# Optimization experiments

Measured on AMD Instinct MI355X. Metric: run time of the kernel, lower is better.

Reference implementation:

```python
import jax, jax.numpy as jnp
import numpy as np

DIM = 256
H = 4
D = DIM // H  # head_dim = 64
SCALE = D ** -0.5


def setup_inputs() -> dict:
    key = jax.random.key(0)
    ks = jax.random.split(key, 12)
    B, N, M = 4, 2048, 2048
    x_query = jax.random.normal(ks[0], (B, N, DIM), dtype=jnp.float32)
    x_context = jax.random.normal(ks[1], (B, M, DIM), dtype=jnp.float32)
    geo_bias = jax.random.normal(ks[2], (B, H, N, M), dtype=jnp.float32)
    init = 1.0 / np.sqrt(DIM)
    Wq = jax.random.uniform(ks[3], (DIM, DIM), jnp.float32, -init, init)
    bq = jax.random.uniform(ks[4], (DIM,), jnp.float32, -init, init)
    Wk = jax.random.uniform(ks[5], (DIM, DIM), jnp.float32, -init, init)
    bk = jax.random.uniform(ks[6], (DIM,), jnp.float32, -init, init)
    Wv = jax.random.uniform(ks[7], (DIM, DIM), jnp.float32, -init, init)
    bv = jax.random.uniform(ks[8], (DIM,), jnp.float32, -init, init)
    Wo = jax.random.uniform(ks[9], (DIM, DIM), jnp.float32, -init, init)
    bo = jax.random.uniform(ks[10], (DIM,), jnp.float32, -init, init)
    return {"x_query": x_query, "x_context": x_context, "geo_bias": geo_bias,
            "Wq": Wq, "bq": bq, "Wk": Wk, "bk": bk, "Wv": Wv, "bv": bv,
            "Wo": Wo, "bo": bo}


def reference(x_query, x_context, geo_bias, Wq, bq, Wk, bk, Wv, bv, Wo, bo):
    B, N, _ = x_query.shape
    M = x_context.shape[1]
    # projections; nn.Linear computes x @ W.T + b
    q = (x_query @ Wq.T + bq).reshape(B, N, H, D).transpose(0, 2, 1, 3)   # (B,H,N,D)
    k = (x_context @ Wk.T + bk).reshape(B, M, H, D).transpose(0, 2, 1, 3)  # (B,H,M,D)
    v = (x_context @ Wv.T + bv).reshape(B, M, H, D).transpose(0, 2, 1, 3)  # (B,H,M,D)
    attn = jnp.einsum("bhnd,bhmd->bhnm", q, k) * SCALE + geo_bias
    attn = jax.nn.softmax(attn, axis=-1)
    out = jnp.einsum("bhnm,bhmd->bhnd", attn, v)
    out = out.transpose(0, 2, 1, 3).reshape(B, N, DIM)
    return out @ Wo.T + bo
```

## Files before the change

### kernel.cpp

```cpp
#include <hip/hip_runtime.h>

typedef unsigned short u16;
typedef unsigned int u32;
using bf16x8  = __attribute__((ext_vector_type(8))) __bf16;
using u16x8   = __attribute__((ext_vector_type(8), may_alias)) u16;
using u16x4   = __attribute__((ext_vector_type(4), may_alias)) u16;
using f32x4   = __attribute__((ext_vector_type(4))) float;
using f32x4_a = __attribute__((ext_vector_type(4), may_alias)) float;

#define DEV __device__ __forceinline__

constexpr int Bn = 4, Hn = 4, Nn = 2048, Mn = 2048, Dn = 64, DIMn = 256;
constexpr float SCALEc = 0.125f;
constexpr float SHIFTc = 12.0f;
constexpr int LSTRIDE = 152;

DEV float bf2f(u16 h) { u32 u = ((u32)h) << 16; return __builtin_bit_cast(float, u); }
DEV u16 f2bf(float f) {
    u32 u = __builtin_bit_cast(u32, f);
    u += 0x7fffu + ((u >> 16) & 1u);
    return (u16)(u >> 16);
}
DEV bf16x8 ld8bf(const u16* p) {
    return __builtin_bit_cast(bf16x8, *reinterpret_cast<const u16x8*>(p));
}
DEV bf16x8 ld8f_bf(const float* p) {
    const f32x4 a = *reinterpret_cast<const f32x4_a*>(p);
    const f32x4 b = *reinterpret_cast<const f32x4_a*>(p + 4);
    u16x8 r;
    r[0] = f2bf(a[0]); r[1] = f2bf(a[1]); r[2] = f2bf(a[2]); r[3] = f2bf(a[3]);
    r[4] = f2bf(b[0]); r[5] = f2bf(b[1]); r[6] = f2bf(b[2]); r[7] = f2bf(b[3]);
    return __builtin_bit_cast(bf16x8, r);
}

__global__ __launch_bounds__(256, 4) void qkv_kernel(
    const float* __restrict__ Xq, const float* __restrict__ Wq, const float* __restrict__ bq,
    const float* __restrict__ Xc, const float* __restrict__ Wk, const float* __restrict__ bk,
    const float* __restrict__ Wv, const float* __restrict__ bv,
    float* __restrict__ Q, u16* __restrict__ K, u16* __restrict__ V)
{
    const int wave = threadIdx.x >> 6, lane = threadIdx.x & 63;
    const int quad = lane >> 4, l16 = lane & 15;
    const int o0 = wave * 64;

    if (blockIdx.x < 512) {
        const int row0 = blockIdx.x * 16;
        const int b = row0 >> 11, n0 = row0 & 2047;
        f32x4 acc[4] = {};
        #pragma unroll
        for (int k0 = 0; k0 < 256; k0 += 32) {
            bf16x8 wf[4];
            const bf16x8 af = ld8f_bf(Xq + (size_t)(row0 + l16) * DIMn + k0 + quad * 8);
            #pragma unroll
            for (int os = 0; os < 4; os++)
                wf[os] = ld8f_bf(Wq + (size_t)(o0 + os * 16 + l16) * DIMn + k0 + quad * 8);
            #pragma unroll
            for (int os = 0; os < 4; os++)
                acc[os] = __builtin_amdgcn_mfma_f32_16x16x32_bf16(af, wf[os], acc[os], 0, 0, 0);
        }
        #pragma unroll
        for (int os = 0; os < 4; os++) {
            const int col = o0 + os * 16 + l16;
            const int h = col >> 6, d = col & 63;
            const float bb = bq[col];
            #pragma unroll
            for (int r = 0; r < 4; r++) {
                const int n = n0 + quad * 4 + r;
                Q[((size_t)(b * Hn + h) * Nn + n) * Dn + d] = acc[os][r] + bb;
            }
        }
    } else {
        const int row0 = (blockIdx.x - 512) * 16;
        const int b = row0 >> 11, n0 = row0 & 2047;
        f32x4 ack[4] = {};
        f32x4 acv[4] = {};
        #pragma unroll
        for (int k0 = 0; k0 < 256; k0 += 32) {
            bf16x8 wkf[4], wvf[4];
            const bf16x8 af = ld8f_bf(Xc + (size_t)(row0 + l16) * DIMn + k0 + quad * 8);
            #pragma unroll
            for (int os = 0; os < 4; os++) {
                wkf[os] = ld8f_bf(Wk + (size_t)(o0 + os * 16 + l16) * DIMn + k0 + quad * 8);
                wvf[os] = ld8f_bf(Wv + (size_t)(o0 + os * 16 + l16) * DIMn + k0 + quad * 8);
            }
            #pragma unroll
            for (int os = 0; os < 4; os++) {
                ack[os] = __builtin_amdgcn_mfma_f32_16x16x32_bf16(af, wkf[os], ack[os], 0, 0, 0);
                acv[os] = __builtin_amdgcn_mfma_f32_16x16x32_bf16(wvf[os], af, acv[os], 0, 0, 0);
            }
        }
        #pragma unroll
        for (int os = 0; os < 4; os++) {
            const int col = o0 + os * 16 + l16;
            const int h = col >> 6, d = col & 63;
            const float bb = bk[col];
            #pragma unroll
            for (int r = 0; r < 4; r++) {
                const int m = n0 + quad * 4 + r;
                K[((size_t)(b * Hn + h) * Mn + m) * Dn + d] = f2bf(ack[os][r] + bb);
            }
        }
        #pragma unroll
        for (int os = 0; os < 4; os++)
            #pragma unroll
            for (int r = 0; r < 4; r++) {
                const int colf = o0 + os * 16 + quad * 4 + r;
                const int h = colf >> 6, d = colf & 63;
                const float bb = bv[colf];
                const int m = n0 + l16;
                V[((size_t)(b * Hn + h) * Dn + d) * Mn + m] = f2bf(acv[os][r] + bb);
            }
    }
}

__global__ __launch_bounds__(256, 4) void attn_kernel(
    const float* __restrict__ Q,
    const u16* __restrict__ K,
    const u16* __restrict__ V,
    const float* __restrict__ geo,
    float* __restrict__ Pnum,
    float* __restrict__ Lsum,
    int S)
{
    __shared__ __align__(16) u16 lds[4][32 * LSTRIDE];

    const int h = blockIdx.y;
    const int b = blockIdx.z / S, split = blockIdx.z % S;
    const int wave = threadIdx.x >> 6, lane = threadIdx.x & 63;
    const int quad = lane >> 4, l16 = lane & 15;
    const int nbase = blockIdx.x * 128 + wave * 32;
    const int mlen = Mn / S, mbeg = split * mlen;

    const float* Qh = Q + ((size_t)(b * Hn + h) * Nn + nbase) * Dn;
    const u16*   Kh = K + (size_t)(b * Hn + h) * Mn * Dn;
    const u16*   Vh = V + (size_t)(b * Hn + h) * Dn * Mn;
    const float* Gq0 = geo + ((size_t)(b * Hn + h) * Nn + nbase + l16) * (size_t)Mn + quad * 4;
    const float* Gq1 = Gq0 + (size_t)16 * Mn;

    bf16x8 qh[2][2], ql[2][2];
    #pragma unroll
    for (int nt = 0; nt < 2; nt++)
        #pragma unroll
        for (int kh = 0; kh < 2; kh++) {
            const float* qp = Qh + (size_t)(nt * 16 + l16) * Dn + kh * 32 + quad * 8;
            const f32x4 a = *reinterpret_cast<const f32x4_a*>(qp);
            const f32x4 c = *reinterpret_cast<const f32x4_a*>(qp + 4);
            u16x8 hi, lo;
            #pragma unroll
            for (int j = 0; j < 4; j++) {
                hi[j] = f2bf(a[j]); lo[j] = f2bf(a[j] - bf2f(hi[j]));
                hi[4 + j] = f2bf(c[j]); lo[4 + j] = f2bf(c[j] - bf2f(hi[4 + j]));
            }
            qh[nt][kh] = __builtin_bit_cast(bf16x8, hi);
            ql[nt][kh] = __builtin_bit_cast(bf16x8, lo);
        }

    f32x4 oacc[2][4] = {};
    float lsum0 = 0.f, lsum1 = 0.f;
    u16* pl = &lds[wave][0];
    const u16* kbase = Kh + (size_t)l16 * Dn + quad * 8;

    for (int m0 = mbeg; m0 < mbeg + mlen; m0 += 128) {
        const u16* kp0 = kbase + (size_t)m0 * Dn;
        bf16x8 kb0 = ld8bf(kp0), kb1 = ld8bf(kp0 + 32);
        f32x4 g0 = *reinterpret_cast<const f32x4_a*>(Gq0 + m0);
        f32x4 g1 = *reinterpret_cast<const f32x4_a*>(Gq1 + m0);
        #pragma unroll
        for (int ms = 0; ms < 8; ms++) {
            bf16x8 nk0, nk1; f32x4 ng0, ng1;
            if (ms < 7) {
                const int mb = m0 + (ms + 1) * 16;
                const u16* kp = kbase + (size_t)mb * Dn;
                nk0 = ld8bf(kp); nk1 = ld8bf(kp + 32);
                ng0 = *reinterpret_cast<const f32x4_a*>(Gq0 + mb);
                ng1 = *reinterpret_cast<const f32x4_a*>(Gq1 + mb);
            }
            f32x4 s0 = {}, s1 = {};
            __builtin_amdgcn_s_setprio(1);
            s0 = __builtin_amdgcn_mfma_f32_16x16x32_bf16(kb0, qh[0][0], s0, 0, 0, 0);
            s1 = __builtin_amdgcn_mfma_f32_16x16x32_bf16(kb0, qh[1][0], s1, 0, 0, 0);
            s0 = __builtin_amdgcn_mfma_f32_16x16x32_bf16(kb0, ql[0][0], s0, 0, 0, 0);
            s1 = __builtin_amdgcn_mfma_f32_16x16x32_bf16(kb0, ql[1][0], s1, 0, 0, 0);
            s0 = __builtin_amdgcn_mfma_f32_16x16x32_bf16(kb1, qh[0][1], s0, 0, 0, 0);
            s1 = __builtin_amdgcn_mfma_f32_16x16x32_bf16(kb1, qh[1][1], s1, 0, 0, 0);
            s0 = __builtin_amdgcn_mfma_f32_16x16x32_bf16(kb1, ql[0][1], s0, 0, 0, 0);
            s1 = __builtin_amdgcn_mfma_f32_16x16x32_bf16(kb1, ql[1][1], s1, 0, 0, 0);
            __builtin_amdgcn_s_setprio(0);
            u16x4 pk0, pk1;
            float ls0 = 0.f, ls1 = 0.f;
            #pragma unroll
            for (int r = 0; r < 4; r++) {
                const float p0 = __expf(fmaf(s0[r], SCALEc, g0[r]) - SHIFTc);
                const float p1 = __expf(fmaf(s1[r], SCALEc, g1[r]) - SHIFTc);
                ls0 += p0; ls1 += p1;
                pk0[r] = f2bf(p0); pk1[r] = f2bf(p1);
            }
            lsum0 += ls0; lsum1 += ls1;
            *reinterpret_cast<u16x4*>(pl + l16 * LSTRIDE + ms * 16 + quad * 4) = pk0;
            *reinterpret_cast<u16x4*>(pl + (16 + l16) * LSTRIDE + ms * 16 + quad * 4) = pk1;
            if (ms < 7) { kb0 = nk0; kb1 = nk1; g0 = ng0; g1 = ng1; }
        }
        const u16* vb0 = Vh + (size_t)l16 * Mn + m0 + quad * 8;
        #pragma unroll
        for (int kh = 0; kh < 4; kh++) {
            const bf16x8 pa0 = ld8bf(pl + l16 * LSTRIDE + kh * 32 + quad * 8);
            const bf16x8 pa1 = ld8bf(pl + (16 + l16) * LSTRIDE + kh * 32 + quad * 8);
            bf16x8 vb[4];
            #pragma unroll
            for (int ds = 0; ds < 4; ds++)
                vb[ds] = ld8bf(vb0 + (size_t)(ds * 16) * Mn + kh * 32);
            __builtin_amdgcn_s_setprio(1);
            #pragma unroll
            for (int ds = 0; ds < 4; ds++) {
                oacc[0][ds] = __builtin_amdgcn_mfma_f32_16x16x32_bf16(pa0, vb[ds], oacc[0][ds], 0, 0, 0);
                oacc[1][ds] = __builtin_amdgcn_mfma_f32_16x16x32_bf16(pa1, vb[ds], oacc[1][ds], 0, 0, 0);
            }
            __builtin_amdgcn_s_setprio(0);
        }
    }

    lsum0 += __shfl_xor(lsum0, 16);
    lsum0 += __shfl_xor(lsum0, 32);
    lsum1 += __shfl_xor(lsum1, 16);
    lsum1 += __shfl_xor(lsum1, 32);

    float* PN = Pnum + (size_t)split * (Bn * (size_t)Nn * DIMn)
                     + ((size_t)b * Nn + nbase) * DIMn + h * Dn;
    #pragma unroll
    for (int nt = 0; nt < 2; nt++)
        #pragma unroll
        for (int r = 0; r < 4; r++)
            #pragma unroll
            for (int ds = 0; ds < 4; ds++)
                PN[(size_t)(nt * 16 + quad * 4 + r) * DIMn + ds * 16 + l16] = oacc[nt][ds][r];

    if (lane < 16) {
        Lsum[(((size_t)split * Bn + b) * Hn + h) * Nn + nbase + l16] = lsum0;
        Lsum[(((size_t)split * Bn + b) * Hn + h) * Nn + nbase + 16 + l16] = lsum1;
    }
}

__global__ __launch_bounds__(256) void combine_kernel(
    const float* __restrict__ Pnum, const float* __restrict__ Lsum,
    u16* __restrict__ AO, int S)
{
    const int idx = blockIdx.x * 256 + threadIdx.x;
    const int row = idx >> 5;
    const int c0  = (idx & 31) * 8;
    const int b = row >> 11, n = row & 2047, h = c0 >> 6;

    float l = 0.f;
    for (int s = 0; s < S; s++)
        l += Lsum[(((size_t)s * Bn + b) * Hn + h) * Nn + n];
    const float inv = 1.0f / l;

    f32x4 a0 = {}, a1 = {};
    for (int s = 0; s < S; s++) {
        const float* p = Pnum + (size_t)s * (Bn * (size_t)Nn * DIMn) + (size_t)row * DIMn + c0;
        a0 += *reinterpret_cast<const f32x4_a*>(p);
        a1 += *reinterpret_cast<const f32x4_a*>(p + 4);
    }
    u16x8 o;
    #pragma unroll
    for (int j = 0; j < 4; j++) {
        o[j]     = f2bf(a0[j] * inv);
        o[4 + j] = f2bf(a1[j] * inv);
    }
    *reinterpret_cast<u16x8*>(AO + (size_t)row * DIMn + c0) = o;
}

__global__ __launch_bounds__(256, 4) void oproj_kernel(
    const u16* __restrict__ A, const float* __restrict__ W,
    const float* __restrict__ bias, float* __restrict__ out)
{
    const int row0 = blockIdx.x * 16;
    const int wave = threadIdx.x >> 6, lane = threadIdx.x & 63;
    const int quad = lane >> 4, l16 = lane & 15;
    const int o0 = wave * 64;

    f32x4 acc[4] = {};
    #pragma unroll
    for (int k0 = 0; k0 < 256; k0 += 32) {
        bf16x8 wf[4];
        const bf16x8 af = ld8bf(A + (size_t)(row0 + l16) * DIMn + k0 + quad * 8);
        #pragma unroll
        for (int os = 0; os < 4; os++)
            wf[os] = ld8f_bf(W + (size_t)(o0 + os * 16 + l16) * DIMn + k0 + quad * 8);
        #pragma unroll
        for (int os = 0; os < 4; os++)
            acc[os] = __builtin_amdgcn_mfma_f32_16x16x32_bf16(af, wf[os], acc[os], 0, 0, 0);
    }
    #pragma unroll
    for (int os = 0; os < 4; os++) {
        const int col = o0 + os * 16 + l16;
        const float bb = bias[col];
        #pragma unroll
        for (int r = 0; r < 4; r++) {
            const int row = row0 + quad * 4 + r;
            out[(size_t)row * DIMn + col] = acc[os][r] + bb;
        }
    }
}

extern "C" void kernel_launch(void* const* d_in, const int* in_sizes, int n_in,
                              void* d_out, int out_size, void* d_ws, size_t ws_size,
                              hipStream_t stream) {
    const float* xq  = (const float*)d_in[0];
    const float* xc  = (const float*)d_in[1];
    const float* geo = (const float*)d_in[2];
    const float* Wq  = (const float*)d_in[3];
    const float* bq  = (const float*)d_in[4];
    const float* Wk  = (const float*)d_in[5];
    const float* bk  = (const float*)d_in[6];
    const float* Wv  = (const float*)d_in[7];
    const float* bv  = (const float*)d_in[8];
    const float* Wo  = (const float*)d_in[9];
    const float* bo  = (const float*)d_in[10];

    const int S = (ws_size >= (60ull << 20)) ? 4 : 1;

    char* ws = (char*)d_ws;
    float* Qw   = (float*)ws;
    u16*   Kw   = (u16*)(ws + (8ull << 20));
    u16*   Vw   = (u16*)(ws + (12ull << 20));
    u16*   AOw  = (u16*)(ws + (16ull << 20));
    float* Pnum = (float*)(ws + (20ull << 20));
    float* Lsum = (float*)(ws + (20ull << 20) + (size_t)S * (8ull << 20));

    qkv_kernel<<<1024, 256, 0, stream>>>(xq, Wq, bq, xc, Wk, bk, Wv, bv, Qw, Kw, Vw);
    attn_kernel<<<dim3(Nn / 128, Hn, Bn * S), 256, 0, stream>>>(Qw, Kw, Vw, geo, Pnum, Lsum, S);
    combine_kernel<<<(Bn * Nn * 32) / 256, 256, 0, stream>>>(Pnum, Lsum, AOw, S);
    oproj_kernel<<<Bn * Nn / 16, 256, 0, stream>>>(AOw, Wo, bo, (float*)d_out);
}
```

Before: 569.4 us.

## Shrink attention tile to 16 rows per wave and fuse split-combine into output projection

The attention kernel now gives each wave 16 query rows instead of 32, which doubles the grid and halves the registers and LDS each block needs. The geo-bias loads for a whole 128-column chunk are now issued in one batch ahead of use. The separate combine kernel is removed: the output projection reads the split partial numerators and sums directly, normalises them and converts them to bf16 in registers. This saves one launch and the AO round trip through memory. In exchange, each K/V tile is loaded twice as often per query row, and the oproj kernel repeats the split reduction for each k-slice.

```diff
diff --git a/kernel.cpp b/kernel.cpp
--- a/kernel.cpp
+++ b/kernel.cpp
@@ -122,170 +122,154 @@
     float* __restrict__ Lsum,
     int S)
 {
-    __shared__ __align__(16) u16 lds[4][32 * LSTRIDE];
+    __shared__ __align__(16) u16 lds[4][16 * LSTRIDE];
 
     const int h = blockIdx.y;
     const int b = blockIdx.z / S, split = blockIdx.z % S;
     const int wave = threadIdx.x >> 6, lane = threadIdx.x & 63;
     const int quad = lane >> 4, l16 = lane & 15;
-    const int nbase = blockIdx.x * 128 + wave * 32;
-    const int mlen = Mn / S, mbeg = split * mlen;
+    const int nbase = blockIdx.x * 64 + wave * 16;
+    const int mlen = Mn / S, mbeg = split * mlen, mend = mbeg + mlen;
 
     const float* Qh = Q + ((size_t)(b * Hn + h) * Nn + nbase) * Dn;
     const u16*   Kh = K + (size_t)(b * Hn + h) * Mn * Dn;
     const u16*   Vh = V + (size_t)(b * Hn + h) * Dn * Mn;
-    const float* Gq0 = geo + ((size_t)(b * Hn + h) * Nn + nbase + l16) * (size_t)Mn + quad * 4;
-    const float* Gq1 = Gq0 + (size_t)16 * Mn;
-
-    bf16x8 qh[2][2], ql[2][2];
-    #pragma unroll
-    for (int nt = 0; nt < 2; nt++)
-        #pragma unroll
-        for (int kh = 0; kh < 2; kh++) {
-            const float* qp = Qh + (size_t)(nt * 16 + l16) * Dn + kh * 32 + quad * 8;
-            const f32x4 a = *reinterpret_cast<const f32x4_a*>(qp);
-            const f32x4 c = *reinterpret_cast<const f32x4_a*>(qp + 4);
-            u16x8 hi, lo;
-            #pragma unroll
-            for (int j = 0; j < 4; j++) {
-                hi[j] = f2bf(a[j]); lo[j] = f2bf(a[j] - bf2f(hi[j]));
-                hi[4 + j] = f2bf(c[j]); lo[4 + j] = f2bf(c[j] - bf2f(hi[4 + j]));
-            }
-            qh[nt][kh] = __builtin_bit_cast(bf16x8, hi);
-            ql[nt][kh] = __builtin_bit_cast(bf16x8, lo);
-        }
-
-    f32x4 oacc[2][4] = {};
-    float lsum0 = 0.f, lsum1 = 0.f;
+    const float* Gl = geo + ((size_t)(b * Hn + h) * Nn + nbase + l16) * (size_t)Mn + quad * 4;
+
+    bf16x8 qh[2], ql[2];
+    #pragma unroll
+    for (int kh = 0; kh < 2; kh++) {
+        const float* qp = Qh + (size_t)l16 * Dn + kh * 32 + quad * 8;
+        const f32x4 a = *reinterpret_cast<const f32x4_a*>(qp);
+        const f32x4 c = *reinterpret_cast<const f32x4_a*>(qp + 4);
+        u16x8 hi, lo;
+        #pragma unroll
+        for (int j = 0; j < 4; j++) {
+            hi[j] = f2bf(a[j]); lo[j] = f2bf(a[j] - bf2f(hi[j]));
+            hi[4 + j] = f2bf(c[j]); lo[4 + j] = f2bf(c[j] - bf2f(hi[4 + j]));
+        }
+        qh[kh] = __builtin_bit_cast(bf16x8, hi);
+        ql[kh] = __builtin_bit_cast(bf16x8, lo);
+    }
+
+    f32x4 oacc[4] = {};
+    float lsum = 0.f;
     u16* pl = &lds[wave][0];
     const u16* kbase = Kh + (size_t)l16 * Dn + quad * 8;
-
-    for (int m0 = mbeg; m0 < mbeg + mlen; m0 += 128) {
-        const u16* kp0 = kbase + (size_t)m0 * Dn;
-        bf16x8 kb0 = ld8bf(kp0), kb1 = ld8bf(kp0 + 32);
-        f32x4 g0 = *reinterpret_cast<const f32x4_a*>(Gq0 + m0);
-        f32x4 g1 = *reinterpret_cast<const f32x4_a*>(Gq1 + m0);
+    const u16* vbase = Vh + (size_t)l16 * Mn + quad * 8;
+
+    f32x4 g[8];
+    #pragma unroll
+    for (int ms = 0; ms < 8; ms++)
+        g[ms] = *reinterpret_cast<const f32x4_a*>(Gl + mbeg + ms * 16);
+    bf16x8 kb0 = ld8bf(kbase + (size_t)mbeg * Dn);
+    bf16x8 kb1 = ld8bf(kbase + (size_t)mbeg * Dn + 32);
+
+    for (int m0 = mbeg; m0 < mend; m0 += 128) {
         #pragma unroll
         for (int ms = 0; ms < 8; ms++) {
-            bf16x8 nk0, nk1; f32x4 ng0, ng1;
-            if (ms < 7) {
-                const int mb = m0 + (ms + 1) * 16;
-                const u16* kp = kbase + (size_t)mb * Dn;
-                nk0 = ld8bf(kp); nk1 = ld8bf(kp + 32);
-                ng0 = *reinterpret_cast<const f32x4_a*>(Gq0 + mb);
-                ng1 = *reinterpret_cast<const f32x4_a*>(Gq1 + mb);
-            }
-            f32x4 s0 = {}, s1 = {};
+            int mb = m0 + (ms + 1) * 16;
+            if (mb > mend - 16) mb = mend - 16;
+            const u16* kp = kbase + (size_t)mb * Dn;
+            const bf16x8 nk0 = ld8bf(kp);
+            const bf16x8 nk1 = ld8bf(kp + 32);
+            f32x4 s = {};
             __builtin_amdgcn_s_setprio(1);
-            s0 = __builtin_amdgcn_mfma_f32_16x16x32_bf16(kb0, qh[0][0], s0, 0, 0, 0);
-            s1 = __builtin_amdgcn_mfma_f32_16x16x32_bf16(kb0, qh[1][0], s1, 0, 0, 0);
-            s0 = __builtin_amdgcn_mfma_f32_16x16x32_bf16(kb0, ql[0][0], s0, 0, 0, 0);
-            s1 = __builtin_amdgcn_mfma_f32_16x16x32_bf16(kb0, ql[1][0], s1, 0, 0, 0);
-            s0 = __builtin_amdgcn_mfma_f32_16x16x32_bf16(kb1, qh[0][1], s0, 0, 0, 0);
-            s1 = __builtin_amdgcn_mfma_f32_16x16x32_bf16(kb1, qh[1][1], s1, 0, 0, 0);
-            s0 = __builtin_amdgcn_mfma_f32_16x16x32_bf16(kb1, ql[0][1], s0, 0, 0, 0);
-            s1 = __builtin_amdgcn_mfma_f32_16x16x32_bf16(kb1, ql[1][1], s1, 0, 0, 0);
+            s = __builtin_amdgcn_mfma_f32_16x16x32_bf16(kb0, qh[0], s, 0, 0, 0);
+            s = __builtin_amdgcn_mfma_f32_16x16x32_bf16(kb0, ql[0], s, 0, 0, 0);
+            s = __builtin_amdgcn_mfma_f32_16x16x32_bf16(kb1, qh[1], s, 0, 0, 0);
+            s = __builtin_amdgcn_mfma_f32_16x16x32_bf16(kb1, ql[1], s, 0, 0, 0);
             __builtin_amdgcn_s_setprio(0);
-            u16x4 pk0, pk1;
-            float ls0 = 0.f, ls1 = 0.f;
+            u16x4 pk;
+            float ls = 0.f;
             #pragma unroll
             for (int r = 0; r < 4; r++) {
-                const float p0 = __expf(fmaf(s0[r], SCALEc, g0[r]) - SHIFTc);
-                const float p1 = __expf(fmaf(s1[r], SCALEc, g1[r]) - SHIFTc);
-                ls0 += p0; ls1 += p1;
-                pk0[r] = f2bf(p0); pk1[r] = f2bf(p1);
-            }
-            lsum0 += ls0; lsum1 += ls1;
-            *reinterpret_cast<u16x4*>(pl + l16 * LSTRIDE + ms * 16 + quad * 4) = pk0;
-            *reinterpret_cast<u16x4*>(pl + (16 + l16) * LSTRIDE + ms * 16 + quad * 4) = pk1;
-            if (ms < 7) { kb0 = nk0; kb1 = nk1; g0 = ng0; g1 = ng1; }
-        }
-        const u16* vb0 = Vh + (size_t)l16 * Mn + m0 + quad * 8;
+                const float p = __expf(fmaf(s[r], SCALEc, g[ms][r]) - SHIFTc);
+                ls += p;
+                pk[r] = f2bf(p);
+            }
+            lsum += ls;
+            *reinterpret_cast<u16x4*>(pl + l16 * LSTRIDE + ms * 16 + quad * 4) = pk;
+            kb0 = nk0; kb1 = nk1;
+        }
+        if (m0 + 128 < mend) {
+            #pragma unroll
+            for (int ms = 0; ms < 8; ms++)
+                g[ms] = *reinterpret_cast<const f32x4_a*>(Gl + m0 + 128 + ms * 16);
+        }
         #pragma unroll
         for (int kh = 0; kh < 4; kh++) {
-            const bf16x8 pa0 = ld8bf(pl + l16 * LSTRIDE + kh * 32 + quad * 8);
-            const bf16x8 pa1 = ld8bf(pl + (16 + l16) * LSTRIDE + kh * 32 + quad * 8);
+            const bf16x8 pa = ld8bf(pl + l16 * LSTRIDE + kh * 32 + quad * 8);
             bf16x8 vb[4];
             #pragma unroll
             for (int ds = 0; ds < 4; ds++)
-                vb[ds] = ld8bf(vb0 + (size_t)(ds * 16) * Mn + kh * 32);
+                vb[ds] = ld8bf(vbase + (size_t)(ds * 16) * Mn + m0 + kh * 32);
             __builtin_amdgcn_s_setprio(1);
             #pragma unroll
-            for (int ds = 0; ds < 4; ds++) {
-                oacc[0][ds] = __builtin_amdgcn_mfma_f32_16x16x32_bf16(pa0, vb[ds], oacc[0][ds], 0, 0, 0);
-                oacc[1][ds] = __builtin_amdgcn_mfma_f32_16x16x32_bf16(pa1, vb[ds], oacc[1][ds], 0, 0, 0);
-            }
+            for (int ds = 0; ds < 4; ds++)
+                oacc[ds] = __builtin_amdgcn_mfma_f32_16x16x32_bf16(pa, vb[ds], oacc[ds], 0, 0, 0);
             __builtin_amdgcn_s_setprio(0);
         }
     }
 
-    lsum0 += __shfl_xor(lsum0, 16);
-    lsum0 += __shfl_xor(lsum0, 32);
-    lsum1 += __shfl_xor(lsum1, 16);
-    lsum1 += __shfl_xor(lsum1, 32);
+    lsum += __shfl_xor(lsum, 16);
+    lsum += __shfl_xor(lsum, 32);
 
     float* PN = Pnum + (size_t)split * (Bn * (size_t)Nn * DIMn)
                      + ((size_t)b * Nn + nbase) * DIMn + h * Dn;
     #pragma unroll
-    for (int nt = 0; nt < 2; nt++)
-        #pragma unroll
-        for (int r = 0; r < 4; r++)
-            #pragma unroll
-            for (int ds = 0; ds < 4; ds++)
-                PN[(size_t)(nt * 16 + quad * 4 + r) * DIMn + ds * 16 + l16] = oacc[nt][ds][r];
-
-    if (lane < 16) {
-        Lsum[(((size_t)split * Bn + b) * Hn + h) * Nn + nbase + l16] = lsum0;
-        Lsum[(((size_t)split * Bn + b) * Hn + h) * Nn + nbase + 16 + l16] = lsum1;
-    }
-}
-
-__global__ __launch_bounds__(256) void combine_kernel(
+    for (int r = 0; r < 4; r++)
+        #pragma unroll
+        for (int ds = 0; ds < 4; ds++)
+            PN[(size_t)(quad * 4 + r) * DIMn + ds * 16 + l16] = oacc[ds][r];
+
+    if (lane < 16)
+        Lsum[(((size_t)split * Bn + b) * Hn + h) * Nn + nbase + l16] = lsum;
+}
+
+__global__ __launch_bounds__(256, 4) void oproj_kernel(
     const float* __restrict__ Pnum, const float* __restrict__ Lsum,
-    u16* __restrict__ AO, int S)
-{
-    const int idx = blockIdx.x * 256 + threadIdx.x;
-    const int row = idx >> 5;
-    const int c0  = (idx & 31) * 8;
-    const int b = row >> 11, n = row & 2047, h = c0 >> 6;
-
-    float l = 0.f;
-    for (int s = 0; s < S; s++)
-        l += Lsum[(((size_t)s * Bn + b) * Hn + h) * Nn + n];
-    const float inv = 1.0f / l;
-
-    f32x4 a0 = {}, a1 = {};
-    for (int s = 0; s < S; s++) {
-        const float* p = Pnum + (size_t)s * (Bn * (size_t)Nn * DIMn) + (size_t)row * DIMn + c0;
-        a0 += *reinterpret_cast<const f32x4_a*>(p);
-        a1 += *reinterpret_cast<const f32x4_a*>(p + 4);
-    }
-    u16x8 o;
-    #pragma unroll
-    for (int j = 0; j < 4; j++) {
-        o[j]     = f2bf(a0[j] * inv);
-        o[4 + j] = f2bf(a1[j] * inv);
-    }
-    *reinterpret_cast<u16x8*>(AO + (size_t)row * DIMn + c0) = o;
-}
-
-__global__ __launch_bounds__(256, 4) void oproj_kernel(
-    const u16* __restrict__ A, const float* __restrict__ W,
-    const float* __restrict__ bias, float* __restrict__ out)
+    const float* __restrict__ W, const float* __restrict__ bias,
+    float* __restrict__ out, int S)
 {
     const int row0 = blockIdx.x * 16;
     const int wave = threadIdx.x >> 6, lane = threadIdx.x & 63;
     const int quad = lane >> 4, l16 = lane & 15;
     const int o0 = wave * 64;
+    const size_t slab = (size_t)Bn * Nn * DIMn;
+
+    const int arow = row0 + l16;
+    const int b = arow >> 11, n = arow & 2047;
+    float inv[4];
+    #pragma unroll
+    for (int hh = 0; hh < 4; hh++) {
+        float l = 0.f;
+        for (int s = 0; s < S; s++)
+            l += Lsum[(((size_t)s * Bn + b) * Hn + hh) * Nn + n];
+        inv[hh] = 1.0f / l;
+    }
 
     f32x4 acc[4] = {};
     #pragma unroll
     for (int k0 = 0; k0 < 256; k0 += 32) {
         bf16x8 wf[4];
-        const bf16x8 af = ld8bf(A + (size_t)(row0 + l16) * DIMn + k0 + quad * 8);
         #pragma unroll
         for (int os = 0; os < 4; os++)
             wf[os] = ld8f_bf(W + (size_t)(o0 + os * 16 + l16) * DIMn + k0 + quad * 8);
+        f32x4 a0 = {}, a1 = {};
+        for (int s = 0; s < S; s++) {
+            const float* p = Pnum + (size_t)s * slab + (size_t)arow * DIMn + k0 + quad * 8;
+            a0 += *reinterpret_cast<const f32x4_a*>(p);
+            a1 += *reinterpret_cast<const f32x4_a*>(p + 4);
+        }
+        const float iv = inv[(k0 + quad * 8) >> 6];
+        u16x8 r;
+        #pragma unroll
+        for (int j = 0; j < 4; j++) {
+            r[j]     = f2bf(a0[j] * iv);
+            r[4 + j] = f2bf(a1[j] * iv);
+        }
+        const bf16x8 af = __builtin_bit_cast(bf16x8, r);
         #pragma unroll
         for (int os = 0; os < 4; os++)
             acc[os] = __builtin_amdgcn_mfma_f32_16x16x32_bf16(af, wf[os], acc[os], 0, 0, 0);
@@ -323,12 +307,10 @@
     float* Qw   = (float*)ws;
     u16*   Kw   = (u16*)(ws + (8ull << 20));
     u16*   Vw   = (u16*)(ws + (12ull << 20));
-    u16*   AOw  = (u16*)(ws + (16ull << 20));
     float* Pnum = (float*)(ws + (20ull << 20));
     float* Lsum = (float*)(ws + (20ull << 20) + (size_t)S * (8ull << 20));
 
     qkv_kernel<<<1024, 256, 0, stream>>>(xq, Wq, bq, xc, Wk, bk, Wv, bv, Qw, Kw, Vw);
-    attn_kernel<<<dim3(Nn / 128, Hn, Bn * S), 256, 0, stream>>>(Qw, Kw, Vw, geo, Pnum, Lsum, S);
-    combine_kernel<<<(Bn * Nn * 32) / 256, 256, 0, stream>>>(Pnum, Lsum, AOw, S);
-    oproj_kernel<<<Bn * Nn / 16, 256, 0, stream>>>(AOw, Wo, bo, (float*)d_out);
-}
+    attn_kernel<<<dim3(Nn / 64, Hn, Bn * S), 256, 0, stream>>>(Qw, Kw, Vw, geo, Pnum, Lsum, S);
+    oproj_kernel<<<Bn * Nn / 16, 256, 0, stream>>>(Pnum, Lsum, Wo, bo, (float*)d_out, S);
+}
```

New measurement: 561.3 us. About the same (-1.4%).
